# Kernel optimization log

Hardware: AMD Instinct MI355X
Metric: run time of the kernel (lower is better)

## Reference

```python
import jax, jax.numpy as jnp
import numpy as np
from jax import lax

B, C, T = 16, 1, 1048576
LEVEL = 5
SELECTED = (3, 4, 5)  # indices into [h1,h2,h3,h4,h5,lowpass5]

SYM4_LO = np.array([-0.07576571478927333, -0.02963552764599851, 0.49761866763201545,
                    0.8037387518059161, 0.29785779560527736, -0.09921954357684722,
                    -0.012603967262037833, 0.032223100604071304], dtype=np.float32)
SYM4_HI = np.array([-0.032223100604071304, -0.012603967262037833, 0.09921954357684722,
                    0.29785779560527736, -0.8037387518059161, 0.49761866763201545,
                    0.02963552764599851, -0.07576571478927333], dtype=np.float32)


def setup_inputs() -> dict:
    key = jax.random.key(0)
    x = jax.random.normal(key, (B, C, T), dtype=jnp.float32)
    return {"x": x, "lowpass": jnp.asarray(SYM4_LO), "highpass": jnp.asarray(SYM4_HI)}


def _circ_conv(x, w):
    # torch: circular pad by L//2 each side, then valid cross-correlation (conv1d).
    pad = w.shape[0] // 2  # 4 for sym4
    xp = jnp.pad(x, ((0, 0), (0, 0), (pad, pad)), mode="wrap")  # (B,1,T+2*pad)
    # lax conv is cross-correlation (no kernel flip), matching torch conv1d.
    return lax.conv_general_dilated(
        xp, w[None, None, :].astype(x.dtype), window_strides=(1,),
        padding="VALID", dimension_numbers=("NCH", "OIH", "NCH"))  # (B,1,T+1)


def reference(x, lowpass, highpass):
    T_in = x.shape[-1]
    coeffs = []
    cur = x
    for _ in range(LEVEL):  # fixed small level loop, not a data-dim loop
        lo = _circ_conv(cur, lowpass)[..., :T_in]
        hi = _circ_conv(cur, highpass)[..., :T_in]
        coeffs.append(hi)
        cur = lo
    coeffs.append(cur[..., :T_in])  # final lowpass approximation
    # include_lowpass=True: pop(-1)+append(-1) is a no-op on ordering.
    out = jnp.stack([coeffs[i] for i in SELECTED], axis=2)  # (B,1,3,T)
    return out
```

## Files before the change

kernel.cpp:

```cpp
#include <hip/hip_runtime.h>


#define TILE 1024
#define NCHUNK ((TILE + 36) / 4)

static constexpr float SYM4_LO[8] = {
    -0.07576571478927333f, -0.02963552764599851f, 0.49761866763201545f,
     0.8037387518059161f,   0.29785779560527736f, -0.09921954357684722f,
    -0.012603967262037833f, 0.032223100604071304f};
static constexpr float SYM4_HI[8] = {
    -0.032223100604071304f, -0.012603967262037833f, 0.09921954357684722f,
     0.29785779560527736f,  -0.8037387518059161f,   0.49761866763201545f,
     0.02963552764599851f,  -0.07576571478927333f};

struct FiltPack {
    float f4[36];
    float f5[36];
    float fl[36];
};

constexpr FiltPack make_filters() {
    double lo[8], hi[8];
    for (int i = 0; i < 8; ++i) { lo[i] = SYM4_LO[i]; hi[i] = SYM4_HI[i]; }
    double l2[15] = {}, l3[22] = {}, l4[29] = {};
    for (int i = 0; i < 8;  ++i) for (int j = 0; j < 8; ++j) l2[i + j] += lo[i] * lo[j];
    for (int i = 0; i < 15; ++i) for (int j = 0; j < 8; ++j) l3[i + j] += l2[i] * lo[j];
    for (int i = 0; i < 22; ++i) for (int j = 0; j < 8; ++j) l4[i + j] += l3[i] * lo[j];
    double f4[29] = {}, f5[36] = {}, fl[36] = {};
    for (int i = 0; i < 22; ++i) for (int j = 0; j < 8; ++j) f4[i + j] += l3[i] * hi[j];
    for (int i = 0; i < 29; ++i) for (int j = 0; j < 8; ++j) f5[i + j] += l4[i] * hi[j];
    for (int i = 0; i < 29; ++i) for (int j = 0; j < 8; ++j) fl[i + j] += l4[i] * lo[j];
    FiltPack r = {};
    for (int m = 0; m < 36; ++m) {
        r.f4[m] = (m >= 4 && m < 33) ? (float)f4[m - 4] : 0.0f;
        r.f5[m] = (float)f5[m];
        r.fl[m] = (float)fl[m];
    }
    return r;
}
static constexpr FiltPack FP = make_filters();

__global__ __launch_bounds__(256)
void modwt_fused_kernel(const float* __restrict__ x, float* __restrict__ out, int Tn) {
    const int T4  = Tn >> 2;
    const int b   = blockIdx.y;
    const int bs4 = blockIdx.x * (TILE / 4);

    __shared__ float4 s4[NCHUNK];

    const float4* x4 = reinterpret_cast<const float4*>(x) + (size_t)b * T4;
    for (int i = threadIdx.x; i < NCHUNK; i += 256) {
        int g = bs4 - 5 + i;
        if (g < 0)    g += T4;
        if (g >= T4)  g -= T4;
        s4[i] = x4[g];
    }
    __syncthreads();

    float w[40];
    #pragma unroll
    for (int j = 0; j < 10; ++j)
        reinterpret_cast<float4*>(w)[j] = s4[threadIdx.x + j];

    float a4[4] = {0.f, 0.f, 0.f, 0.f};
    float a5[4] = {0.f, 0.f, 0.f, 0.f};
    float al[4] = {0.f, 0.f, 0.f, 0.f};
    #pragma unroll
    for (int m = 0; m < 36; ++m) {
        const float c4 = FP.f4[m];
        const float c5 = FP.f5[m];
        const float cl = FP.fl[m];
        #pragma unroll
        for (int j = 0; j < 4; ++j) {
            const float xv = w[m + j];
            a4[j] = fmaf(c4, xv, a4[j]);
            a5[j] = fmaf(c5, xv, a5[j]);
            al[j] = fmaf(cl, xv, al[j]);
        }
    }

    float4* o4 = reinterpret_cast<float4*>(out);
    const size_t base = (size_t)b * 3 * T4 + bs4 + threadIdx.x;
    o4[base]                 = make_float4(a4[0], a4[1], a4[2], a4[3]);
    o4[base + T4]            = make_float4(a5[0], a5[1], a5[2], a5[3]);
    o4[base + 2 * (size_t)T4] = make_float4(al[0], al[1], al[2], al[3]);
}

extern "C" void kernel_launch(void* const* d_in, const int* in_sizes, int n_in,
                              void* d_out, int out_size, void* d_ws, size_t ws_size,
                              hipStream_t stream) {
    const float* x = (const float*)d_in[0];
    float* out = (float*)d_out;
    const int B  = 16;
    const int Tn = in_sizes[0] / B;

    dim3 grid(Tn / TILE, B);
    dim3 block(256);
    modwt_fused_kernel<<<grid, block, 0, stream>>>(x, out, Tn);
}
```

Measured before the change: 59.41 us.

## Make blocks persistent over several tiles with register-prefetched next tile

Each block now handles eight tiles in a grid-stride loop, prefetching the next tile's input into registers while the current tile is computed from shared memory. Outputs use nontemporal stores, and zero taps of the f4 filter are skipped at compile time. The aim is to hide global load latency and cut the cost of launching many short blocks. In exchange the grid has fewer blocks, which may lower occupancy or parallelism, and each tile now needs two barriers.

```diff
diff --git a/kernel.cpp b/kernel.cpp
--- a/kernel.cpp
+++ b/kernel.cpp
@@ -1,8 +1,11 @@
 #include <hip/hip_runtime.h>
 
 
-#define TILE 1024
-#define NCHUNK ((TILE + 36) / 4)
+#define TILE      1024
+#define NCHUNK    265
+#define TPB_TILES 8
+
+typedef float f4v __attribute__((ext_vector_type(4)));
 
 static constexpr float SYM4_LO[8] = {
     -0.07576571478927333f, -0.02963552764599851f, 0.49761866763201545f,
@@ -41,49 +44,80 @@
 static constexpr FiltPack FP = make_filters();
 
 __global__ __launch_bounds__(256)
-void modwt_fused_kernel(const float* __restrict__ x, float* __restrict__ out, int Tn) {
+void modwt_fused_kernel(const float* __restrict__ x, float* __restrict__ out,
+                        int Tn, int tilesPerRow, int totalTiles) {
     const int T4  = Tn >> 2;
-    const int b   = blockIdx.y;
-    const int bs4 = blockIdx.x * (TILE / 4);
+    const int tid = threadIdx.x;
+    const bool have2 = (tid < NCHUNK - 256);
 
-    __shared__ float4 s4[NCHUNK];
+    __shared__ f4v s4[NCHUNK];
 
-    const float4* x4 = reinterpret_cast<const float4*>(x) + (size_t)b * T4;
-    for (int i = threadIdx.x; i < NCHUNK; i += 256) {
-        int g = bs4 - 5 + i;
-        if (g < 0)    g += T4;
-        if (g >= T4)  g -= T4;
-        s4[i] = x4[g];
-    }
-    __syncthreads();
+    const f4v* xbase = reinterpret_cast<const f4v*>(x);
+    f4v* o4 = reinterpret_cast<f4v*>(out);
 
-    float w[40];
-    #pragma unroll
-    for (int j = 0; j < 10; ++j)
-        reinterpret_cast<float4*>(w)[j] = s4[threadIdx.x + j];
+    int tile = blockIdx.x;
 
-    float a4[4] = {0.f, 0.f, 0.f, 0.f};
-    float a5[4] = {0.f, 0.f, 0.f, 0.f};
-    float al[4] = {0.f, 0.f, 0.f, 0.f};
-    #pragma unroll
-    for (int m = 0; m < 36; ++m) {
-        const float c4 = FP.f4[m];
-        const float c5 = FP.f5[m];
-        const float cl = FP.fl[m];
-        #pragma unroll
-        for (int j = 0; j < 4; ++j) {
-            const float xv = w[m + j];
-            a4[j] = fmaf(c4, xv, a4[j]);
-            a5[j] = fmaf(c5, xv, a5[j]);
-            al[j] = fmaf(cl, xv, al[j]);
-        }
+    f4v c0, c1;
+    {
+        const int b   = tile / tilesPerRow;
+        const int bs4 = (tile % tilesPerRow) * (TILE / 4);
+        const f4v* xr = xbase + (size_t)b * T4;
+        int g0 = bs4 - 5 + tid;           if (g0 < 0)   g0 += T4;
+        c0 = xr[g0];
+        if (have2) { int g1 = bs4 - 5 + 256 + tid; if (g1 >= T4) g1 -= T4; c1 = xr[g1]; }
     }
 
-    float4* o4 = reinterpret_cast<float4*>(out);
-    const size_t base = (size_t)b * 3 * T4 + bs4 + threadIdx.x;
-    o4[base]                 = make_float4(a4[0], a4[1], a4[2], a4[3]);
-    o4[base + T4]            = make_float4(a5[0], a5[1], a5[2], a5[3]);
-    o4[base + 2 * (size_t)T4] = make_float4(al[0], al[1], al[2], al[3]);
+    for (int k = 0; k < TPB_TILES; ++k) {
+        const int b   = tile / tilesPerRow;
+        const int bs4 = (tile % tilesPerRow) * (TILE / 4);
+
+        __syncthreads();
+        s4[tid] = c0;
+        if (have2) s4[256 + tid] = c1;
+
+        const int ntile = tile + gridDim.x;
+        if (ntile < totalTiles) {
+            const int nb   = ntile / tilesPerRow;
+            const int nbs4 = (ntile % tilesPerRow) * (TILE / 4);
+            const f4v* xr = xbase + (size_t)nb * T4;
+            int g0 = nbs4 - 5 + tid;          if (g0 < 0)   g0 += T4;
+            c0 = xr[g0];
+            if (have2) { int g1 = nbs4 - 5 + 256 + tid; if (g1 >= T4) g1 -= T4; c1 = xr[g1]; }
+        }
+        __syncthreads();
+
+        float w[40];
+        #pragma unroll
+        for (int j = 0; j < 10; ++j)
+            reinterpret_cast<f4v*>(w)[j] = s4[tid + j];
+
+        float a4[4] = {0.f, 0.f, 0.f, 0.f};
+        float a5[4] = {0.f, 0.f, 0.f, 0.f};
+        float al[4] = {0.f, 0.f, 0.f, 0.f};
+        #pragma unroll
+        for (int m = 0; m < 36; ++m) {
+            const float c4v = FP.f4[m];
+            const float c5v = FP.f5[m];
+            const float clv = FP.fl[m];
+            #pragma unroll
+            for (int j = 0; j < 4; ++j) {
+                const float xv = w[m + j];
+                if (c4v != 0.0f) a4[j] = fmaf(c4v, xv, a4[j]);
+                a5[j] = fmaf(c5v, xv, a5[j]);
+                al[j] = fmaf(clv, xv, al[j]);
+            }
+        }
+
+        const size_t base = ((size_t)b * 3) * T4 + bs4 + tid;
+        f4v v4 = {a4[0], a4[1], a4[2], a4[3]};
+        f4v v5 = {a5[0], a5[1], a5[2], a5[3]};
+        f4v vl = {al[0], al[1], al[2], al[3]};
+        __builtin_nontemporal_store(v4, &o4[base]);
+        __builtin_nontemporal_store(v5, &o4[base + T4]);
+        __builtin_nontemporal_store(vl, &o4[base + 2 * (size_t)T4]);
+
+        tile = ntile;
+    }
 }
 
 extern "C" void kernel_launch(void* const* d_in, const int* in_sizes, int n_in,
@@ -93,8 +127,10 @@
     float* out = (float*)d_out;
     const int B  = 16;
     const int Tn = in_sizes[0] / B;
+    const int tilesPerRow = Tn / TILE;
+    const int totalTiles  = B * tilesPerRow;
 
-    dim3 grid(Tn / TILE, B);
+    dim3 grid(totalTiles / TPB_TILES);
     dim3 block(256);
-    modwt_fused_kernel<<<grid, block, 0, stream>>>(x, out, Tn);
+    modwt_fused_kernel<<<grid, block, 0, stream>>>(x, out, Tn, tilesPerRow, totalTiles);
 }
```

New measurement: 52.79 us. -11.1%, faster.
